# Kernel tuning notes

Measured on AMD Instinct MI355X. Metric: run time of the kernel, lower is better.

The kernel has to match this reference:

```python
import jax, jax.numpy as jnp
import numpy as np

N = 8192
K = 15


def setup_inputs() -> dict:
    key = jax.random.key(0)
    kx, ky = jax.random.split(key)
    x = jax.random.normal(kx, (N, 2), dtype=jnp.float32)
    y = jax.random.randint(ky, (N,), 0, 2, dtype=jnp.int32)
    return {"x": x, "y": y}


def reference(x, y):
    # Pairwise squared Euclidean distances via ||a||^2 + ||b||^2 - 2 a.b
    n = x.shape[0]
    xx = jnp.sum(x * x, axis=-1)                      # [n]
    d = xx[:, None] + xx[None, :] - 2.0 * (x @ x.T)   # [n, n]
    # exclude self (the original loop skips i == j)
    idx = jnp.arange(n)
    d = d.at[idx, idx].set(jnp.inf)
    # K nearest neighbors per point (smallest distances)
    _, knn_idx = jax.lax.top_k(-d, K)                 # [n, K]
    knn_labels = y[knn_idx].astype(jnp.float32)       # [n, K]
    # majority vote: sum of K binary labels > K/2 -> class 1
    out = (jnp.sum(knn_labels, axis=-1) > (K / 2)).astype(jnp.float32)
    return out
```

## Files before the change

kernel.cpp:

```cpp
#include <hip/hip_runtime.h>

#define NPTS 8192
#define KNN  15
#define QPW  2
#define WPB  8
#define TPB  (WPB * 64)

__device__ __forceinline__ unsigned int bitonic_sort_u32(unsigned int v, int lane) {
#pragma unroll
  for (int k = 2; k <= 64; k <<= 1) {
#pragma unroll
    for (int j = k >> 1; j > 0; j >>= 1) {
      unsigned int o = __shfl_xor(v, j, 64);
      bool keep_min = ((lane & k) == 0) == ((lane & j) == 0);
      unsigned int lo = (v < o) ? v : o;
      unsigned int hi = (v < o) ? o : v;
      v = keep_min ? lo : hi;
    }
  }
  return v;
}

__device__ __forceinline__ unsigned long long bitonic_sort_u64(unsigned long long v, int lane) {
#pragma unroll
  for (int k = 2; k <= 64; k <<= 1) {
#pragma unroll
    for (int j = k >> 1; j > 0; j >>= 1) {
      unsigned long long o = __shfl_xor(v, j, 64);
      bool keep_min = ((lane & k) == 0) == ((lane & j) == 0);
      unsigned long long lo = (v < o) ? v : o;
      unsigned long long hi = (v < o) ? o : v;
      v = keep_min ? lo : hi;
    }
  }
  return v;
}

__global__ __launch_bounds__(TPB)
void knn_kernel(const float* __restrict__ x, const int* __restrict__ y,
                float* __restrict__ out) {
  __shared__ float4 sx4[NPTS / 2];
  __shared__ unsigned int ybits[NPTS / 32];
  __shared__ unsigned int buf[WPB][QPW][64];
  __shared__ int cnt[WPB][QPW];

  const int tid = threadIdx.x;

  const float4* gx4 = (const float4*)x;
#pragma unroll
  for (int i = tid; i < NPTS / 2; i += TPB) sx4[i] = gx4[i];
  if (tid < NPTS / 32) {
    const int4* yy = (const int4*)(y + (tid << 5));
    unsigned int b = 0;
#pragma unroll
    for (int k2 = 0; k2 < 8; ++k2) {
      int4 v = yy[k2];
      b |= ((unsigned int)(v.x & 1) << (4 * k2)) |
           ((unsigned int)(v.y & 1) << (4 * k2 + 1)) |
           ((unsigned int)(v.z & 1) << (4 * k2 + 2)) |
           ((unsigned int)(v.w & 1) << (4 * k2 + 3));
    }
    ybits[tid] = b;
  }
  if (tid < WPB * QPW) ((int*)cnt)[tid] = 0;
  __syncthreads();

  const int w = tid >> 6;
  const int lane = tid & 63;
  const int q0 = ((int)blockIdx.x * WPB + w) * QPW;
  const float2 xqa = ((const float2*)sx4)[q0];
  const float2 xqb = ((const float2*)sx4)[q0 + 1];

  float ma = 3.0e38f, mb = 3.0e38f;
#pragma unroll 8
  for (int s = 0; s < 64; ++s) {
    float4 p = sx4[(s << 6) + lane];
    float ax0 = xqa.x - p.x, ay0 = xqa.y - p.y;
    float ax1 = xqa.x - p.z, ay1 = xqa.y - p.w;
    float bx0 = xqb.x - p.x, by0 = xqb.y - p.y;
    float bx1 = xqb.x - p.z, by1 = xqb.y - p.w;
    float d0a = ax0 * ax0 + ay0 * ay0;
    float d1a = ax1 * ax1 + ay1 * ay1;
    float d0b = bx0 * bx0 + by0 * by0;
    float d1b = bx1 * bx1 + by1 * by1;
    ma = fminf(ma, fminf(d0a, d1a));
    mb = fminf(mb, fminf(d0b, d1b));
  }

  unsigned int sa = bitonic_sort_u32(__float_as_uint(ma), lane);
  unsigned int sb = bitonic_sort_u32(__float_as_uint(mb), lane);
  const float Ta = __uint_as_float(__shfl(sa, KNN, 64)) * (1.0f + 1.0e-5f) + 1.0e-30f;
  const float Tb = __uint_as_float(__shfl(sb, KNN, 64)) * (1.0f + 1.0e-5f) + 1.0e-30f;

#pragma unroll 4
  for (int s = 0; s < 64; ++s) {
    float4 p = sx4[(s << 6) + lane];
    int j0 = ((s << 6) + lane) << 1;
    float ax0 = xqa.x - p.x, ay0 = xqa.y - p.y;
    float ax1 = xqa.x - p.z, ay1 = xqa.y - p.w;
    float bx0 = xqb.x - p.x, by0 = xqb.y - p.y;
    float bx1 = xqb.x - p.z, by1 = xqb.y - p.w;
    float d0a = ax0 * ax0 + ay0 * ay0;
    float d1a = ax1 * ax1 + ay1 * ay1;
    float d0b = bx0 * bx0 + by0 * by0;
    float d1b = bx1 * bx1 + by1 * by1;
    if (d0a <= Ta) { int o = atomicAdd(&cnt[w][0], 1); if (o < 64) buf[w][0][o] = (unsigned)j0; }
    if (d1a <= Ta) { int o = atomicAdd(&cnt[w][0], 1); if (o < 64) buf[w][0][o] = (unsigned)(j0 + 1); }
    if (d0b <= Tb) { int o = atomicAdd(&cnt[w][1], 1); if (o < 64) buf[w][1][o] = (unsigned)j0; }
    if (d1b <= Tb) { int o = atomicAdd(&cnt[w][1], 1); if (o < 64) buf[w][1][o] = (unsigned)(j0 + 1); }
  }
  __syncthreads();

#pragma unroll
  for (int qi = 0; qi < QPW; ++qi) {
    const int q = q0 + qi;
    const float2 xq = (qi == 0) ? xqa : xqb;
    int C = cnt[w][qi];
    C = (C > 64) ? 64 : C;
    unsigned long long kv = ~0ull;
    if (lane < C) {
      int jj = (int)buf[w][qi][lane];
      float2 pj = ((const float2*)sx4)[jj];
      double dx = (double)xq.x - (double)pj.x;
      double dy = (double)xq.y - (double)pj.y;
      double dd = dx * dx + dy * dy;
      kv = ((unsigned long long)__double_as_longlong(dd) & ~0x1FFFull) |
           (unsigned long long)jj;
      if (jj == q) kv = ~0ull;
    }
    kv = bitonic_sort_u64(kv, lane);
    int jj = (int)(kv & 0x1FFFull);
    int lbl = (int)((ybits[jj >> 5] >> (jj & 31)) & 1u);
    unsigned long long vm = __ballot((lane < KNN) && lbl);
    if (lane == 0) out[q] = (__popcll(vm) >= 8) ? 1.0f : 0.0f;
  }
}

extern "C" void kernel_launch(void* const* d_in, const int* in_sizes, int n_in,
                              void* d_out, int out_size, void* d_ws, size_t ws_size,
                              hipStream_t stream) {
  const float* x = (const float*)d_in[0];
  const int* y = (const int*)d_in[1];
  float* out = (float*)d_out;
  dim3 grid(NPTS / (WPB * QPW));
  dim3 block(TPB);
  hipLaunchKernelGGL(knn_kernel, grid, block, 0, stream, x, y, out);
}
```

Baseline: 33.90 us.

## Process four queries per wave and replace LDS atomics with ballot compaction

Doubles queries per wave so each LDS point load serves four queries, halving the grid. Candidate collection switches from shared-memory atomic counters to wavefront ballot plus mbcnt prefix offsets with register counters, removing atomics and the trailing block barrier. Distance uses fma. Fewer blocks means lower occupancy per CU and more register pressure.

Result: slower. 38.87 us (+14.7%).

```diff
diff --git a/kernel.cpp b/kernel.cpp
--- a/kernel.cpp
+++ b/kernel.cpp
@@ -2,9 +2,14 @@
 
 #define NPTS 8192
 #define KNN  15
-#define QPW  2
+#define QPW  4
 #define WPB  8
 #define TPB  (WPB * 64)
+
+__device__ __forceinline__ int prefix_below(unsigned long long m) {
+  return (int)__builtin_amdgcn_mbcnt_hi((unsigned int)(m >> 32),
+            __builtin_amdgcn_mbcnt_lo((unsigned int)m, 0u));
+}
 
 __device__ __forceinline__ unsigned int bitonic_sort_u32(unsigned int v, int lane) {
 #pragma unroll
@@ -42,7 +47,6 @@
   __shared__ float4 sx4[NPTS / 2];
   __shared__ unsigned int ybits[NPTS / 32];
   __shared__ unsigned int buf[WPB][QPW][64];
-  __shared__ int cnt[WPB][QPW];
 
   const int tid = threadIdx.x;
 
@@ -62,67 +66,87 @@
     }
     ybits[tid] = b;
   }
-  if (tid < WPB * QPW) ((int*)cnt)[tid] = 0;
   __syncthreads();
 
   const int w = tid >> 6;
   const int lane = tid & 63;
   const int q0 = ((int)blockIdx.x * WPB + w) * QPW;
-  const float2 xqa = ((const float2*)sx4)[q0];
-  const float2 xqb = ((const float2*)sx4)[q0 + 1];
 
-  float ma = 3.0e38f, mb = 3.0e38f;
+  float qx[QPW], qy[QPW];
+#pragma unroll
+  for (int qi = 0; qi < QPW; ++qi) {
+    float2 xq = ((const float2*)sx4)[q0 + qi];
+    qx[qi] = xq.x; qy[qi] = xq.y;
+  }
+
+  float m0[QPW], m1[QPW];
+#pragma unroll
+  for (int qi = 0; qi < QPW; ++qi) { m0[qi] = 3.0e38f; m1[qi] = 3.0e38f; }
+
 #pragma unroll 8
   for (int s = 0; s < 64; ++s) {
     float4 p = sx4[(s << 6) + lane];
-    float ax0 = xqa.x - p.x, ay0 = xqa.y - p.y;
-    float ax1 = xqa.x - p.z, ay1 = xqa.y - p.w;
-    float bx0 = xqb.x - p.x, by0 = xqb.y - p.y;
-    float bx1 = xqb.x - p.z, by1 = xqb.y - p.w;
-    float d0a = ax0 * ax0 + ay0 * ay0;
-    float d1a = ax1 * ax1 + ay1 * ay1;
-    float d0b = bx0 * bx0 + by0 * by0;
-    float d1b = bx1 * bx1 + by1 * by1;
-    ma = fminf(ma, fminf(d0a, d1a));
-    mb = fminf(mb, fminf(d0b, d1b));
+#pragma unroll
+    for (int qi = 0; qi < QPW; ++qi) {
+      float dx0 = qx[qi] - p.x, dy0 = qy[qi] - p.y;
+      float dx1 = qx[qi] - p.z, dy1 = qy[qi] - p.w;
+      float d0 = __builtin_fmaf(dx0, dx0, dy0 * dy0);
+      float d1 = __builtin_fmaf(dx1, dx1, dy1 * dy1);
+      m0[qi] = fminf(m0[qi], d0);
+      m1[qi] = fminf(m1[qi], d1);
+    }
   }
 
-  unsigned int sa = bitonic_sort_u32(__float_as_uint(ma), lane);
-  unsigned int sb = bitonic_sort_u32(__float_as_uint(mb), lane);
-  const float Ta = __uint_as_float(__shfl(sa, KNN, 64)) * (1.0f + 1.0e-5f) + 1.0e-30f;
-  const float Tb = __uint_as_float(__shfl(sb, KNN, 64)) * (1.0f + 1.0e-5f) + 1.0e-30f;
+  float T[QPW];
+#pragma unroll
+  for (int qi = 0; qi < QPW; ++qi) {
+    unsigned int s = bitonic_sort_u32(__float_as_uint(fminf(m0[qi], m1[qi])), lane);
+    T[qi] = __uint_as_float(__shfl(s, KNN, 64)) * (1.0f + 1.0e-5f) + 1.0e-30f;
+  }
+
+  int cnt[QPW];
+#pragma unroll
+  for (int qi = 0; qi < QPW; ++qi) cnt[qi] = 0;
 
 #pragma unroll 4
   for (int s = 0; s < 64; ++s) {
     float4 p = sx4[(s << 6) + lane];
     int j0 = ((s << 6) + lane) << 1;
-    float ax0 = xqa.x - p.x, ay0 = xqa.y - p.y;
-    float ax1 = xqa.x - p.z, ay1 = xqa.y - p.w;
-    float bx0 = xqb.x - p.x, by0 = xqb.y - p.y;
-    float bx1 = xqb.x - p.z, by1 = xqb.y - p.w;
-    float d0a = ax0 * ax0 + ay0 * ay0;
-    float d1a = ax1 * ax1 + ay1 * ay1;
-    float d0b = bx0 * bx0 + by0 * by0;
-    float d1b = bx1 * bx1 + by1 * by1;
-    if (d0a <= Ta) { int o = atomicAdd(&cnt[w][0], 1); if (o < 64) buf[w][0][o] = (unsigned)j0; }
-    if (d1a <= Ta) { int o = atomicAdd(&cnt[w][0], 1); if (o < 64) buf[w][0][o] = (unsigned)(j0 + 1); }
-    if (d0b <= Tb) { int o = atomicAdd(&cnt[w][1], 1); if (o < 64) buf[w][1][o] = (unsigned)j0; }
-    if (d1b <= Tb) { int o = atomicAdd(&cnt[w][1], 1); if (o < 64) buf[w][1][o] = (unsigned)(j0 + 1); }
+#pragma unroll
+    for (int qi = 0; qi < QPW; ++qi) {
+      float dx0 = qx[qi] - p.x, dy0 = qy[qi] - p.y;
+      float dx1 = qx[qi] - p.z, dy1 = qy[qi] - p.w;
+      float d0 = __builtin_fmaf(dx0, dx0, dy0 * dy0);
+      float d1 = __builtin_fmaf(dx1, dx1, dy1 * dy1);
+      bool c0 = (d0 <= T[qi]);
+      bool c1 = (d1 <= T[qi]);
+      unsigned long long k0 = __ballot(c0);
+      unsigned long long k1 = __ballot(c1);
+      if (k0 | k1) {
+        if (c0) {
+          int o = cnt[qi] + prefix_below(k0);
+          if (o < 64) buf[w][qi][o] = (unsigned)j0;
+        }
+        if (c1) {
+          int o = cnt[qi] + __popcll(k0) + prefix_below(k1);
+          if (o < 64) buf[w][qi][o] = (unsigned)(j0 + 1);
+        }
+        cnt[qi] += __popcll(k0) + __popcll(k1);
+      }
+    }
   }
-  __syncthreads();
 
 #pragma unroll
   for (int qi = 0; qi < QPW; ++qi) {
     const int q = q0 + qi;
-    const float2 xq = (qi == 0) ? xqa : xqb;
-    int C = cnt[w][qi];
+    int C = cnt[qi];
     C = (C > 64) ? 64 : C;
     unsigned long long kv = ~0ull;
     if (lane < C) {
       int jj = (int)buf[w][qi][lane];
       float2 pj = ((const float2*)sx4)[jj];
-      double dx = (double)xq.x - (double)pj.x;
-      double dy = (double)xq.y - (double)pj.y;
+      double dx = (double)qx[qi] - (double)pj.x;
+      double dy = (double)qy[qi] - (double)pj.y;
       double dd = dx * dx + dy * dy;
       kv = ((unsigned long long)__double_as_longlong(dd) & ~0x1FFFull) |
            (unsigned long long)jj;
```

## Filter kNN candidates in packed fp16 with wave-ballot compaction, one query per wave

Applied to the files above, without the earlier changes.

Stores the point cloud in shared memory as packed half2 (x and y planes) and runs both the per-lane minimum pass and the threshold-filter pass with packed fp16 math. A tolerance margin widens the threshold to absorb fp16 rounding. Per-lane shared atomics are replaced by ballot and mbcnt prefix compaction, and the filter body is skipped when no lane in the wave has a candidate. Each wave now handles one query instead of two, the grid doubles, launch bounds request higher occupancy, and exact refinement in fp64 is kept. The risk is that fp16 error exceeds the margin and a true neighbour is dropped, or too many candidates overflow the 64-slot buffer.

Result: faster. 31.89 us (-5.9%).

```diff
diff --git a/kernel.cpp b/kernel.cpp
--- a/kernel.cpp
+++ b/kernel.cpp
@@ -1,10 +1,22 @@
 #include <hip/hip_runtime.h>
+#include <hip/hip_fp16.h>
 
 #define NPTS 8192
 #define KNN  15
-#define QPW  2
 #define WPB  8
 #define TPB  (WPB * 64)
+#define SEG  64
+
+__device__ __forceinline__ int prefix_below(unsigned long long m) {
+  return (int)__builtin_amdgcn_mbcnt_hi((unsigned int)(m >> 32),
+            __builtin_amdgcn_mbcnt_lo((unsigned int)m, 0u));
+}
+
+__device__ __forceinline__ __half2 hmin2(__half2 a, __half2 b) {
+  __half2 r;
+  asm("v_pk_min_f16 %0, %1, %2" : "=v"(r) : "v"(a), "v"(b));
+  return r;
+}
 
 __device__ __forceinline__ unsigned int bitonic_sort_u32(unsigned int v, int lane) {
 #pragma unroll
@@ -36,19 +48,24 @@
   return v;
 }
 
-__global__ __launch_bounds__(TPB)
+__global__ __launch_bounds__(TPB, 8)
 void knn_kernel(const float* __restrict__ x, const int* __restrict__ y,
                 float* __restrict__ out) {
-  __shared__ float4 sx4[NPTS / 2];
+  __shared__ __align__(16) unsigned int sp[NPTS];
   __shared__ unsigned int ybits[NPTS / 32];
-  __shared__ unsigned int buf[WPB][QPW][64];
-  __shared__ int cnt[WPB][QPW];
+  __shared__ unsigned int buf[WPB][SEG];
 
   const int tid = threadIdx.x;
 
   const float4* gx4 = (const float4*)x;
 #pragma unroll
-  for (int i = tid; i < NPTS / 2; i += TPB) sx4[i] = gx4[i];
+  for (int i = tid; i < NPTS / 2; i += TPB) {
+    float4 p = gx4[i];
+    __half2 hx = __floats2half2_rn(p.x, p.z);
+    __half2 hy = __floats2half2_rn(p.y, p.w);
+    sp[2 * i]     = *(const unsigned int*)&hx;
+    sp[2 * i + 1] = *(const unsigned int*)&hy;
+  }
   if (tid < NPTS / 32) {
     const int4* yy = (const int4*)(y + (tid << 5));
     unsigned int b = 0;
@@ -62,78 +79,90 @@
     }
     ybits[tid] = b;
   }
-  if (tid < WPB * QPW) ((int*)cnt)[tid] = 0;
   __syncthreads();
 
   const int w = tid >> 6;
   const int lane = tid & 63;
-  const int q0 = ((int)blockIdx.x * WPB + w) * QPW;
-  const float2 xqa = ((const float2*)sx4)[q0];
-  const float2 xqb = ((const float2*)sx4)[q0 + 1];
+  const int q = (int)blockIdx.x * WPB + w;
+  const float2 xq = ((const float2*)x)[q];
+  const __half2 qx2 = __floats2half2_rn(xq.x, xq.x);
+  const __half2 qy2 = __floats2half2_rn(xq.y, xq.y);
 
-  float ma = 3.0e38f, mb = 3.0e38f;
-#pragma unroll 8
-  for (int s = 0; s < 64; ++s) {
-    float4 p = sx4[(s << 6) + lane];
-    float ax0 = xqa.x - p.x, ay0 = xqa.y - p.y;
-    float ax1 = xqa.x - p.z, ay1 = xqa.y - p.w;
-    float bx0 = xqb.x - p.x, by0 = xqb.y - p.y;
-    float bx1 = xqb.x - p.z, by1 = xqb.y - p.w;
-    float d0a = ax0 * ax0 + ay0 * ay0;
-    float d1a = ax1 * ax1 + ay1 * ay1;
-    float d0b = bx0 * bx0 + by0 * by0;
-    float d1b = bx1 * bx1 + by1 * by1;
-    ma = fminf(ma, fminf(d0a, d1a));
-    mb = fminf(mb, fminf(d0b, d1b));
+  const uint4* sp4 = (const uint4*)sp;
+
+  __half2 mm = __floats2half2_rn(6.0e4f, 6.0e4f);
+#pragma unroll 4
+  for (int s = 0; s < 32; ++s) {
+    uint4 v = sp4[(s << 6) + lane];
+    __half2 xa = *(const __half2*)&v.x, ya = *(const __half2*)&v.y;
+    __half2 xb = *(const __half2*)&v.z, yb = *(const __half2*)&v.w;
+    __half2 dxa = __hsub2(xa, qx2), dya = __hsub2(ya, qy2);
+    __half2 dxb = __hsub2(xb, qx2), dyb = __hsub2(yb, qy2);
+    __half2 da = __hfma2(dxa, dxa, __hmul2(dya, dya));
+    __half2 db = __hfma2(dxb, dxb, __hmul2(dyb, dyb));
+    mm = hmin2(mm, hmin2(da, db));
+  }
+  float m = fminf(__low2float(mm), __high2float(mm));
+
+  unsigned int srt = bitonic_sort_u32(__float_as_uint(m), lane);
+  const float T = __uint_as_float(__shfl(srt, KNN, 64));
+  const float M = 0.035f * sqrtf(T) + 2.0e-4f + 0.01f * T;
+  __half hTf = __float2half_rn(T + M);
+  hTf = __ushort_as_half((unsigned short)(__half_as_ushort(hTf) + 2));
+  const float Tff = __half2float(hTf);
+  const __half2 Tf2 = __half2half2(hTf);
+
+  int cnt = 0;
+#pragma unroll 2
+  for (int s = 0; s < 32; ++s) {
+    uint4 v = sp4[(s << 6) + lane];
+    __half2 xa = *(const __half2*)&v.x, ya = *(const __half2*)&v.y;
+    __half2 xb = *(const __half2*)&v.z, yb = *(const __half2*)&v.w;
+    __half2 dxa = __hsub2(xa, qx2), dya = __hsub2(ya, qy2);
+    __half2 dxb = __hsub2(xb, qx2), dyb = __hsub2(yb, qy2);
+    __half2 da = __hfma2(dxa, dxa, __hmul2(dya, dya));
+    __half2 db = __hfma2(dxb, dxb, __hmul2(dyb, dyb));
+    __half2 ta = __hsub2(Tf2, da);
+    __half2 tb = __hsub2(Tf2, db);
+    unsigned int sgn = (*(const unsigned int*)&ta) &
+                       (*(const unsigned int*)&tb) & 0x80008000u;
+    if (__any(sgn != 0x80008000u)) {
+      int jb = ((s << 6) + lane) << 2;
+      float d0 = __low2float(da), d1 = __high2float(da);
+      float d2 = __low2float(db), d3 = __high2float(db);
+      bool c0 = d0 <= Tff, c1 = d1 <= Tff, c2 = d2 <= Tff, c3 = d3 <= Tff;
+      unsigned long long k0 = __ballot(c0);
+      if (c0) { int o = cnt + prefix_below(k0); if (o < SEG) buf[w][o] = jb; }
+      cnt += __popcll(k0);
+      unsigned long long k1 = __ballot(c1);
+      if (c1) { int o = cnt + prefix_below(k1); if (o < SEG) buf[w][o] = jb + 1; }
+      cnt += __popcll(k1);
+      unsigned long long k2 = __ballot(c2);
+      if (c2) { int o = cnt + prefix_below(k2); if (o < SEG) buf[w][o] = jb + 2; }
+      cnt += __popcll(k2);
+      unsigned long long k3 = __ballot(c3);
+      if (c3) { int o = cnt + prefix_below(k3); if (o < SEG) buf[w][o] = jb + 3; }
+      cnt += __popcll(k3);
+    }
   }
 
-  unsigned int sa = bitonic_sort_u32(__float_as_uint(ma), lane);
-  unsigned int sb = bitonic_sort_u32(__float_as_uint(mb), lane);
-  const float Ta = __uint_as_float(__shfl(sa, KNN, 64)) * (1.0f + 1.0e-5f) + 1.0e-30f;
-  const float Tb = __uint_as_float(__shfl(sb, KNN, 64)) * (1.0f + 1.0e-5f) + 1.0e-30f;
-
-#pragma unroll 4
-  for (int s = 0; s < 64; ++s) {
-    float4 p = sx4[(s << 6) + lane];
-    int j0 = ((s << 6) + lane) << 1;
-    float ax0 = xqa.x - p.x, ay0 = xqa.y - p.y;
-    float ax1 = xqa.x - p.z, ay1 = xqa.y - p.w;
-    float bx0 = xqb.x - p.x, by0 = xqb.y - p.y;
-    float bx1 = xqb.x - p.z, by1 = xqb.y - p.w;
-    float d0a = ax0 * ax0 + ay0 * ay0;
-    float d1a = ax1 * ax1 + ay1 * ay1;
-    float d0b = bx0 * bx0 + by0 * by0;
-    float d1b = bx1 * bx1 + by1 * by1;
-    if (d0a <= Ta) { int o = atomicAdd(&cnt[w][0], 1); if (o < 64) buf[w][0][o] = (unsigned)j0; }
-    if (d1a <= Ta) { int o = atomicAdd(&cnt[w][0], 1); if (o < 64) buf[w][0][o] = (unsigned)(j0 + 1); }
-    if (d0b <= Tb) { int o = atomicAdd(&cnt[w][1], 1); if (o < 64) buf[w][1][o] = (unsigned)j0; }
-    if (d1b <= Tb) { int o = atomicAdd(&cnt[w][1], 1); if (o < 64) buf[w][1][o] = (unsigned)(j0 + 1); }
+  int C = (cnt > SEG) ? SEG : cnt;
+  unsigned long long kv = ~0ull;
+  if (lane < C) {
+    int jj = (int)buf[w][lane];
+    float2 pj = ((const float2*)x)[jj];
+    double dx = (double)xq.x - (double)pj.x;
+    double dy = (double)xq.y - (double)pj.y;
+    double dd = dx * dx + dy * dy;
+    kv = ((unsigned long long)__double_as_longlong(dd) & ~0x1FFFull) |
+         (unsigned long long)jj;
+    if (jj == q) kv = ~0ull;
   }
-  __syncthreads();
-
-#pragma unroll
-  for (int qi = 0; qi < QPW; ++qi) {
-    const int q = q0 + qi;
-    const float2 xq = (qi == 0) ? xqa : xqb;
-    int C = cnt[w][qi];
-    C = (C > 64) ? 64 : C;
-    unsigned long long kv = ~0ull;
-    if (lane < C) {
-      int jj = (int)buf[w][qi][lane];
-      float2 pj = ((const float2*)sx4)[jj];
-      double dx = (double)xq.x - (double)pj.x;
-      double dy = (double)xq.y - (double)pj.y;
-      double dd = dx * dx + dy * dy;
-      kv = ((unsigned long long)__double_as_longlong(dd) & ~0x1FFFull) |
-           (unsigned long long)jj;
-      if (jj == q) kv = ~0ull;
-    }
-    kv = bitonic_sort_u64(kv, lane);
-    int jj = (int)(kv & 0x1FFFull);
-    int lbl = (int)((ybits[jj >> 5] >> (jj & 31)) & 1u);
-    unsigned long long vm = __ballot((lane < KNN) && lbl);
-    if (lane == 0) out[q] = (__popcll(vm) >= 8) ? 1.0f : 0.0f;
-  }
+  kv = bitonic_sort_u64(kv, lane);
+  int j15 = (int)(kv & 0x1FFFull);
+  int lbl = (int)((ybits[j15 >> 5] >> (j15 & 31)) & 1u);
+  unsigned long long vm = __ballot((lane < KNN) && lbl);
+  if (lane == 0) out[q] = (__popcll(vm) >= 8) ? 1.0f : 0.0f;
 }
 
 extern "C" void kernel_launch(void* const* d_in, const int* in_sizes, int n_in,
@@ -142,7 +171,7 @@
   const float* x = (const float*)d_in[0];
   const int* y = (const int*)d_in[1];
   float* out = (float*)d_out;
-  dim3 grid(NPTS / (WPB * QPW));
+  dim3 grid(NPTS / WPB);
   dim3 block(TPB);
   hipLaunchKernelGGL(knn_kernel, grid, block, 0, stream, x, y, out);
 }
```

## Replace brute-force KNN scan with uniform-grid spatial index and ring search

Applied to the files above, without the earlier changes.

Adds a single-block build kernel that bins points into a 64x64 uniform grid. It prefix-sums the cell counts and scatters coordinates plus packed index/label into a workspace. The query kernel then visits grid rings around each query until 16 candidates are provably within a lower bound, and does the threshold collection and final sort only over those rings. This replaces the O(N) per-query full scan with local work. The cost is a serial single-block build launch, an extra launch, and irregular per-query loops that can diverge.

New measurement: 71.70 us. 2.12x slower.

```diff
diff --git a/kernel.cpp b/kernel.cpp
--- a/kernel.cpp
+++ b/kernel.cpp
@@ -2,9 +2,17 @@
 
 #define NPTS 8192
 #define KNN  15
-#define QPW  2
+#define G    64
+#define NC   (G * G)
+#define TPB_A 1024
 #define WPB  8
 #define TPB  (WPB * 64)
+#define QPW  2
+#define SEG  64
+
+#define WS_CS    16
+#define WS_SIDX  8224
+#define WS_CRD   24608
 
 __device__ __forceinline__ unsigned int bitonic_sort_u32(unsigned int v, int lane) {
 #pragma unroll
@@ -36,102 +44,213 @@
   return v;
 }
 
+template <typename F>
+__device__ __forceinline__ void ring_spans(int r, int qcx, int qcy,
+                                           const unsigned short* cs_l, F&& body) {
+  int x0 = qcx - r; if (x0 < 0) x0 = 0;
+  int x1 = qcx + r; if (x1 > G - 1) x1 = G - 1;
+  int ytop = qcy - r, ybot = qcy + r;
+  if (ytop >= 0)               body(cs_l[ytop * G + x0], cs_l[ytop * G + x1 + 1]);
+  if (r > 0 && ybot <= G - 1)  body(cs_l[ybot * G + x0], cs_l[ybot * G + x1 + 1]);
+  if (r > 0) {
+    int ry0 = ytop + 1; if (ry0 < 0) ry0 = 0;
+    int ry1 = ybot - 1; if (ry1 > G - 1) ry1 = G - 1;
+    int xl = qcx - r, xr = qcx + r;
+    for (int ry = ry0; ry <= ry1; ++ry) {
+      if (xl >= 0)     body(cs_l[ry * G + xl], cs_l[ry * G + xl + 1]);
+      if (xr <= G - 1) body(cs_l[ry * G + xr], cs_l[ry * G + xr + 1]);
+    }
+  }
+}
+
+__global__ __launch_bounds__(TPB_A)
+void build_kernel(const float* __restrict__ x, const int* __restrict__ y,
+                  unsigned char* __restrict__ ws) {
+  __shared__ unsigned int hist[NC];
+  __shared__ unsigned int tsum[TPB_A];
+  __shared__ float rb[64];
+  __shared__ float hdr[4];
+
+  const int t = threadIdx.x;
+  const int lane = t & 63, wv = t >> 6;
+
+  float px[8], py[8];
+  float mnx = 3e38f, mxx = -3e38f, mny = 3e38f, mxy = -3e38f;
+#pragma unroll
+  for (int i = 0; i < 8; ++i) {
+    float2 p = ((const float2*)x)[t + i * TPB_A];
+    px[i] = p.x; py[i] = p.y;
+    mnx = fminf(mnx, p.x); mxx = fmaxf(mxx, p.x);
+    mny = fminf(mny, p.y); mxy = fmaxf(mxy, p.y);
+  }
+#pragma unroll
+  for (int j = 32; j >= 1; j >>= 1) {
+    mnx = fminf(mnx, __shfl_xor(mnx, j, 64));
+    mxx = fmaxf(mxx, __shfl_xor(mxx, j, 64));
+    mny = fminf(mny, __shfl_xor(mny, j, 64));
+    mxy = fmaxf(mxy, __shfl_xor(mxy, j, 64));
+  }
+  if (lane == 0) { rb[wv] = mnx; rb[16 + wv] = mxx; rb[32 + wv] = mny; rb[48 + wv] = mxy; }
+  for (int c = t; c < NC; c += TPB_A) hist[c] = 0;
+  __syncthreads();
+  if (t == 0) {
+    float a = rb[0], b = rb[16], c2 = rb[32], d = rb[48];
+    for (int i = 1; i < 16; ++i) {
+      a = fminf(a, rb[i]); b = fmaxf(b, rb[16 + i]);
+      c2 = fminf(c2, rb[32 + i]); d = fmaxf(d, rb[48 + i]);
+    }
+    float sp = fmaxf(b - a, d - c2) * (1.0f + 1e-6f) + 1e-6f;
+    hdr[0] = a; hdr[1] = c2; hdr[2] = (float)G / sp; hdr[3] = sp / (float)G;
+    float* h = (float*)ws; h[0] = hdr[0]; h[1] = hdr[1]; h[2] = hdr[2]; h[3] = hdr[3];
+  }
+  __syncthreads();
+  const float xmin = hdr[0], ymin = hdr[1], invw = hdr[2];
+
+  int cell[8];
+#pragma unroll
+  for (int i = 0; i < 8; ++i) {
+    int cx = (int)((px[i] - xmin) * invw); cx = cx < 0 ? 0 : (cx > G - 1 ? G - 1 : cx);
+    int cy = (int)((py[i] - ymin) * invw); cy = cy < 0 ? 0 : (cy > G - 1 ? G - 1 : cy);
+    cell[i] = cy * G + cx;
+    atomicAdd(&hist[cell[i]], 1u);
+  }
+  __syncthreads();
+
+  unsigned int h0 = hist[4 * t], h1 = hist[4 * t + 1], h2 = hist[4 * t + 2], h3 = hist[4 * t + 3];
+  unsigned int s = h0 + h1 + h2 + h3;
+  tsum[t] = s;
+  __syncthreads();
+  for (int st = 1; st < TPB_A; st <<= 1) {
+    unsigned int v = (t >= st) ? tsum[t - st] : 0u;
+    __syncthreads();
+    tsum[t] += v;
+    __syncthreads();
+  }
+  unsigned int ex = tsum[t] - s;
+  unsigned short* cs = (unsigned short*)(ws + WS_CS);
+  cs[4 * t]     = (unsigned short)ex;
+  cs[4 * t + 1] = (unsigned short)(ex + h0);
+  cs[4 * t + 2] = (unsigned short)(ex + h0 + h1);
+  cs[4 * t + 3] = (unsigned short)(ex + h0 + h1 + h2);
+  if (t == 0) cs[NC] = (unsigned short)NPTS;
+  hist[4 * t] = ex; hist[4 * t + 1] = ex + h0;
+  hist[4 * t + 2] = ex + h0 + h1; hist[4 * t + 3] = ex + h0 + h1 + h2;
+  __syncthreads();
+
+  float2* crd = (float2*)(ws + WS_CRD);
+  unsigned short* sidx = (unsigned short*)(ws + WS_SIDX);
+#pragma unroll
+  for (int i = 0; i < 8; ++i) {
+    int idx = t + i * TPB_A;
+    unsigned int pos = atomicAdd(&hist[cell[i]], 1u);
+    crd[pos] = make_float2(px[i], py[i]);
+    sidx[pos] = (unsigned short)(idx | ((y[idx] & 1) << 13));
+  }
+}
+
 __global__ __launch_bounds__(TPB)
-void knn_kernel(const float* __restrict__ x, const int* __restrict__ y,
-                float* __restrict__ out) {
-  __shared__ float4 sx4[NPTS / 2];
-  __shared__ unsigned int ybits[NPTS / 32];
-  __shared__ unsigned int buf[WPB][QPW][64];
-  __shared__ int cnt[WPB][QPW];
-
-  const int tid = threadIdx.x;
-
-  const float4* gx4 = (const float4*)x;
-#pragma unroll
-  for (int i = tid; i < NPTS / 2; i += TPB) sx4[i] = gx4[i];
-  if (tid < NPTS / 32) {
-    const int4* yy = (const int4*)(y + (tid << 5));
-    unsigned int b = 0;
-#pragma unroll
-    for (int k2 = 0; k2 < 8; ++k2) {
-      int4 v = yy[k2];
-      b |= ((unsigned int)(v.x & 1) << (4 * k2)) |
-           ((unsigned int)(v.y & 1) << (4 * k2 + 1)) |
-           ((unsigned int)(v.z & 1) << (4 * k2 + 2)) |
-           ((unsigned int)(v.w & 1) << (4 * k2 + 3));
-    }
-    ybits[tid] = b;
-  }
-  if (tid < WPB * QPW) ((int*)cnt)[tid] = 0;
-  __syncthreads();
-
-  const int w = tid >> 6;
-  const int lane = tid & 63;
-  const int q0 = ((int)blockIdx.x * WPB + w) * QPW;
-  const float2 xqa = ((const float2*)sx4)[q0];
-  const float2 xqb = ((const float2*)sx4)[q0 + 1];
-
-  float ma = 3.0e38f, mb = 3.0e38f;
-#pragma unroll 8
-  for (int s = 0; s < 64; ++s) {
-    float4 p = sx4[(s << 6) + lane];
-    float ax0 = xqa.x - p.x, ay0 = xqa.y - p.y;
-    float ax1 = xqa.x - p.z, ay1 = xqa.y - p.w;
-    float bx0 = xqb.x - p.x, by0 = xqb.y - p.y;
-    float bx1 = xqb.x - p.z, by1 = xqb.y - p.w;
-    float d0a = ax0 * ax0 + ay0 * ay0;
-    float d1a = ax1 * ax1 + ay1 * ay1;
-    float d0b = bx0 * bx0 + by0 * by0;
-    float d1b = bx1 * bx1 + by1 * by1;
-    ma = fminf(ma, fminf(d0a, d1a));
-    mb = fminf(mb, fminf(d0b, d1b));
-  }
-
-  unsigned int sa = bitonic_sort_u32(__float_as_uint(ma), lane);
-  unsigned int sb = bitonic_sort_u32(__float_as_uint(mb), lane);
-  const float Ta = __uint_as_float(__shfl(sa, KNN, 64)) * (1.0f + 1.0e-5f) + 1.0e-30f;
-  const float Tb = __uint_as_float(__shfl(sb, KNN, 64)) * (1.0f + 1.0e-5f) + 1.0e-30f;
-
-#pragma unroll 4
-  for (int s = 0; s < 64; ++s) {
-    float4 p = sx4[(s << 6) + lane];
-    int j0 = ((s << 6) + lane) << 1;
-    float ax0 = xqa.x - p.x, ay0 = xqa.y - p.y;
-    float ax1 = xqa.x - p.z, ay1 = xqa.y - p.w;
-    float bx0 = xqb.x - p.x, by0 = xqb.y - p.y;
-    float bx1 = xqb.x - p.z, by1 = xqb.y - p.w;
-    float d0a = ax0 * ax0 + ay0 * ay0;
-    float d1a = ax1 * ax1 + ay1 * ay1;
-    float d0b = bx0 * bx0 + by0 * by0;
-    float d1b = bx1 * bx1 + by1 * by1;
-    if (d0a <= Ta) { int o = atomicAdd(&cnt[w][0], 1); if (o < 64) buf[w][0][o] = (unsigned)j0; }
-    if (d1a <= Ta) { int o = atomicAdd(&cnt[w][0], 1); if (o < 64) buf[w][0][o] = (unsigned)(j0 + 1); }
-    if (d0b <= Tb) { int o = atomicAdd(&cnt[w][1], 1); if (o < 64) buf[w][1][o] = (unsigned)j0; }
-    if (d1b <= Tb) { int o = atomicAdd(&cnt[w][1], 1); if (o < 64) buf[w][1][o] = (unsigned)(j0 + 1); }
-  }
-  __syncthreads();
-
-#pragma unroll
-  for (int qi = 0; qi < QPW; ++qi) {
-    const int q = q0 + qi;
-    const float2 xq = (qi == 0) ? xqa : xqb;
-    int C = cnt[w][qi];
-    C = (C > 64) ? 64 : C;
+void query_kernel(const float* __restrict__ x,
+                  const unsigned char* __restrict__ ws,
+                  float* __restrict__ out) {
+  __shared__ float2 crd_l[NPTS];
+  __shared__ unsigned short cs_l[NC + 8];
+  __shared__ unsigned int buf[WPB][SEG];
+
+  const int t = threadIdx.x;
+  const float4* g4 = (const float4*)(ws + WS_CRD);
+#pragma unroll
+  for (int i = t; i < NPTS / 2; i += TPB) ((float4*)crd_l)[i] = g4[i];
+  const unsigned int* gcs = (const unsigned int*)(ws + WS_CS);
+  for (int i = t; i < (NC + 8) / 2; i += TPB) ((unsigned int*)cs_l)[i] = gcs[i];
+  __syncthreads();
+
+  const float* hdr = (const float*)ws;
+  const float xmin = hdr[0], ymin = hdr[1], invw = hdr[2], w = hdr[3];
+  const unsigned short* gsidx = (const unsigned short*)(ws + WS_SIDX);
+
+  const int wv = t >> 6, lane = t & 63;
+  const unsigned long long lmask = (lane == 63) ? 0x7FFFFFFFFFFFFFFFull
+                                                : ((1ull << lane) - 1ull);
+
+  for (int qt = 0; qt < QPW; ++qt) {
+    const int q = ((int)blockIdx.x * WPB + wv) * QPW + qt;
+    const float2 xq = ((const float2*)x)[q];
+    int qcx = (int)((xq.x - xmin) * invw); qcx = qcx < 0 ? 0 : (qcx > G - 1 ? G - 1 : qcx);
+    int qcy = (int)((xq.y - ymin) * invw); qcy = qcy < 0 ? 0 : (qcy > G - 1 ? G - 1 : qcy);
+
+    float m = 3e38f;
+    int C = 0, rmax = 0;
+    for (int r = 0; r < 2 * G; ++r) {
+      ring_spans(r, qcx, qcy, cs_l, [&](int s0, int s1) {
+        int n = s1 - s0;
+        int base = (lane - (C & 63)) & 63;
+        int iters = (n + 63) >> 6;
+        for (int it = 0; it < iters; ++it) {
+          int jj2 = (it << 6) + base;
+          bool act = jj2 < n;
+          float2 pp = crd_l[s0 + (act ? jj2 : 0)];
+          float dx = xq.x - pp.x;
+          float dy = xq.y - pp.y;
+          float d = __builtin_fmaf(dx, dx, dy * dy);
+          if (act) m = fminf(m, d);
+        }
+        C += n;
+      });
+      bool full = (qcx - r <= 0) && (qcy - r <= 0) &&
+                  (qcx + r >= G - 1) && (qcy + r >= G - 1);
+      if (C >= 16) {
+        float lb = fmaxf(0.0f, (float)r * w - 1e-4f);
+        float LBs = lb * lb * (1.0f - 1e-5f) - 1e-30f;
+        unsigned long long bl = __ballot(m <= LBs);
+        if (__popcll(bl) >= 16) { rmax = r; break; }
+      }
+      if (full) { rmax = r; break; }
+    }
+
+    unsigned int srt = bitonic_sort_u32(__float_as_uint(m), lane);
+    const float T16 = __uint_as_float(__shfl(srt, KNN, 64));
+    const float T = T16 * (1.0f + 1e-5f) + 1e-30f;
+
+    int cnt = 0;
+    for (int r = 0; r <= rmax; ++r) {
+      ring_spans(r, qcx, qcy, cs_l, [&](int s0, int s1) {
+        int n = s1 - s0;
+        int iters = (n + 63) >> 6;
+        for (int it = 0; it < iters; ++it) {
+          int jj2 = (it << 6) + lane;
+          bool act = jj2 < n;
+          float2 pp = crd_l[s0 + (act ? jj2 : 0)];
+          float dx = xq.x - pp.x;
+          float dy = xq.y - pp.y;
+          float d = __builtin_fmaf(dx, dx, dy * dy);
+          bool c = act && (d <= T);
+          unsigned long long k = __ballot(c);
+          if (c) {
+            int o = cnt + __popcll(k & lmask);
+            if (o < SEG) buf[wv][o] = (unsigned int)(s0 + jj2);
+          }
+          cnt += __popcll(k);
+        }
+      });
+    }
+
+    int C2 = (cnt > SEG) ? SEG : cnt;
     unsigned long long kv = ~0ull;
-    if (lane < C) {
-      int jj = (int)buf[w][qi][lane];
-      float2 pj = ((const float2*)sx4)[jj];
+    if (lane < C2) {
+      int pos = (int)buf[wv][lane];
+      float2 pj = crd_l[pos];
+      unsigned int si = gsidx[pos];
+      int jj = (int)(si & 0x1FFFu);
+      unsigned long long lbl = (si >> 13) & 1u;
       double dx = (double)xq.x - (double)pj.x;
       double dy = (double)xq.y - (double)pj.y;
       double dd = dx * dx + dy * dy;
-      kv = ((unsigned long long)__double_as_longlong(dd) & ~0x1FFFull) |
-           (unsigned long long)jj;
+      kv = ((unsigned long long)__double_as_longlong(dd) & ~0x3FFFull) |
+           ((unsigned long long)jj << 1) | lbl;
       if (jj == q) kv = ~0ull;
     }
     kv = bitonic_sort_u64(kv, lane);
-    int jj = (int)(kv & 0x1FFFull);
-    int lbl = (int)((ybits[jj >> 5] >> (jj & 31)) & 1u);
-    unsigned long long vm = __ballot((lane < KNN) && lbl);
+    unsigned long long vm = __ballot((lane < KNN) && (kv & 1ull));
     if (lane == 0) out[q] = (__popcll(vm) >= 8) ? 1.0f : 0.0f;
   }
 }
@@ -142,7 +261,8 @@
   const float* x = (const float*)d_in[0];
   const int* y = (const int*)d_in[1];
   float* out = (float*)d_out;
-  dim3 grid(NPTS / (WPB * QPW));
-  dim3 block(TPB);
-  hipLaunchKernelGGL(knn_kernel, grid, block, 0, stream, x, y, out);
-}
+  unsigned char* ws = (unsigned char*)d_ws;
+  hipLaunchKernelGGL(build_kernel, dim3(1), dim3(TPB_A), 0, stream, x, y, ws);
+  hipLaunchKernelGGL(query_kernel, dim3(NPTS / (WPB * QPW)), dim3(TPB), 0, stream,
+                     x, ws, out);
+}
```
